# Kernel optimization log

Measured on AMD Instinct MI355X. Metric: run time of the kernel, lower is better.

The kernel has to match this reference:

```python
import jax, jax.numpy as jnp
import numpy as np

N = 50000          # nodes
E = 400000         # edges (before self-loops)
F_IN = 64          # node features
H = 256            # hidden_dim
HEADS = 8
HD = 32            # head dim (hidden_dim // 8)
L = 4              # num_layers
G = 64             # num graphs
NGF = 32           # graph features per graph
NC = 2             # classes
EPS = 1e-5


def _bn(x, g, b):
    # BatchNorm1d with batch statistics (training-mode math, no dropout)
    mu = jnp.mean(x, axis=0)
    var = jnp.var(x, axis=0)
    return (x - mu) * jax.lax.rsqrt(var + EPS) * g + b


def _gat(x, src, dst, W, a_src, a_dst, bias):
    # PyG GATConv math (self-loops already included in src/dst)
    h = (x @ W).reshape(N, HEADS, HD)                      # [N,8,32]
    as_n = jnp.sum(h * a_src, axis=-1)                     # [N,8]
    ad_n = jnp.sum(h * a_dst, axis=-1)                     # [N,8]
    e = jax.nn.leaky_relu(as_n[src] + ad_n[dst], 0.2)      # [E',8]
    m = jax.ops.segment_max(e, dst, num_segments=N)        # per-dest softmax
    ex = jnp.exp(e - m[dst])
    den = jax.ops.segment_sum(ex, dst, num_segments=N)
    alpha = ex / den[dst]                                  # [E',8]
    out = jax.ops.segment_sum(alpha[:, :, None] * h[src], dst, num_segments=N)
    return out.reshape(N, HEADS * HD) + bias


def setup_inputs() -> dict:
    key = jax.random.key(0)
    ks = jax.random.split(key, 20)
    s = 0.05
    inp = {
        "x": jax.random.normal(ks[0], (N, F_IN), jnp.float32),
        "edge_index": jax.random.randint(ks[1], (2, E), 0, N, jnp.int32),
        "batch": jnp.sort(jax.random.randint(ks[2], (N,), 0, G, jnp.int32)),
        "graph_features": jax.random.normal(ks[3], (G * NGF,), jnp.float32),
        # node encoder
        "W_enc": jax.random.normal(ks[4], (F_IN, H), jnp.float32) * s,
        "b_enc": jnp.zeros((H,), jnp.float32),
        "g_enc": jnp.ones((H,), jnp.float32),
        "be_enc": jnp.zeros((H,), jnp.float32),
        # GAT layers (stacked over L layers)
        "Wg": jax.random.normal(ks[5], (L, H, H), jnp.float32) * s,
        "att_src": jax.random.normal(ks[6], (L, HEADS, HD), jnp.float32) * s,
        "att_dst": jax.random.normal(ks[7], (L, HEADS, HD), jnp.float32) * s,
        "bg": jnp.zeros((L, H), jnp.float32),
        "bn_g": jnp.ones((L, H), jnp.float32),
        "bn_b": jnp.zeros((L, H), jnp.float32),
        # classifier: (3H + NGF) -> 2H -> H -> NC
        "W1": jax.random.normal(ks[8], (3 * H + NGF, 2 * H), jnp.float32) * s,
        "b1": jnp.zeros((2 * H,), jnp.float32),
        "g1": jnp.ones((2 * H,), jnp.float32),
        "be1": jnp.zeros((2 * H,), jnp.float32),
        "W2": jax.random.normal(ks[9], (2 * H, H), jnp.float32) * s,
        "b2": jnp.zeros((H,), jnp.float32),
        "g2": jnp.ones((H,), jnp.float32),
        "be2": jnp.zeros((H,), jnp.float32),
        "W3": jax.random.normal(ks[10], (H, NC), jnp.float32) * s,
        "b3": jnp.zeros((NC,), jnp.float32),
    }
    return inp


def reference(x, edge_index, batch, graph_features, W_enc, b_enc, g_enc, be_enc,
              Wg, att_src, att_dst, bg, bn_g, bn_b,
              W1, b1, g1, be1, W2, b2, g2, be2, W3, b3):
    gf = graph_features.reshape(G, NGF)
    # add self loops (PyG GATConv default)
    loop = jnp.arange(N, dtype=edge_index.dtype)
    src = jnp.concatenate([edge_index[0], loop])
    dst = jnp.concatenate([edge_index[1], loop])

    h = jax.nn.relu(_bn(x @ W_enc + b_enc, g_enc, be_enc))  # node encoder
    for i in range(L):
        h_in = h
        h = _gat(h, src, dst, Wg[i], att_src[i], att_dst[i], bg[i])
        h = jax.nn.relu(_bn(h, bn_g[i], bn_b[i]))
        if i > 0 and i % 2 == 0:
            h = h + h_in

    # concat pooling: mean / max / sum over graphs
    cnt = jax.ops.segment_sum(jnp.ones((N,), h.dtype), batch, num_segments=G)
    s = jax.ops.segment_sum(h, batch, num_segments=G)
    mean = s / cnt[:, None]
    mx = jax.ops.segment_max(h, batch, num_segments=G)
    pooled = jnp.concatenate([mean, mx, s], axis=1)         # [G, 3H]

    z = jnp.concatenate([pooled, gf], axis=1)               # [G, 3H+NGF]
    z = jax.nn.relu(_bn(z @ W1 + b1, g1, be1))
    z = jax.nn.relu(_bn(z @ W2 + b2, g2, be2))
    return z @ W3 + b3                                      # [G, NC]
```

## Files before the change

### kernel.cpp

```cpp
#include <hip/hip_runtime.h>

#define NN 50000
#define MPAD 50048
#define EE 400000
#define EP 450000
#define FIN 64
#define HH 256
#define GG 64
#define NGFD 32
#define SB 782
#define RB 64

typedef __attribute__((ext_vector_type(8))) _Float16 f16x8;
typedef __attribute__((ext_vector_type(8))) unsigned short u16x8;
typedef __attribute__((ext_vector_type(4))) float f32x4;

__device__ __forceinline__ unsigned short f2h(float f) {
  _Float16 h = (_Float16)f;
  return __builtin_bit_cast(unsigned short, h);
}
__device__ __forceinline__ float h2f(unsigned short s) {
  _Float16 h = __builtin_bit_cast(_Float16, s);
  return (float)h;
}

__global__ void k_init_deg(int* deg) {
  int i = blockIdx.x * 256 + threadIdx.x;
  if (i < NN) deg[i] = 1;
}
__global__ void k_hist(const int* __restrict__ dst, int* __restrict__ deg) {
  int e = blockIdx.x * 256 + threadIdx.x;
  if (e < EE) atomicAdd(&deg[dst[e]], 1);
}
__global__ void k_scan1(const int* __restrict__ deg, int* __restrict__ offs, int* __restrict__ aux) {
  __shared__ int sd[256];
  int b = blockIdx.x, t = threadIdx.x;
  int base = b * 1024 + t * 4;
  int v0 = 0, v1 = 0, v2 = 0, v3 = 0;
  if (base + 0 < NN) v0 = deg[base + 0];
  if (base + 1 < NN) v1 = deg[base + 1];
  if (base + 2 < NN) v2 = deg[base + 2];
  if (base + 3 < NN) v3 = deg[base + 3];
  sd[t] = v0 + v1 + v2 + v3;
  __syncthreads();
  for (int off = 1; off < 256; off <<= 1) {
    int x = (t >= off) ? sd[t - off] : 0;
    __syncthreads();
    sd[t] += x;
    __syncthreads();
  }
  if (t == 255) aux[b] = sd[255];
  int run = (t == 0) ? 0 : sd[t - 1];
  if (base + 0 < NN) offs[base + 0] = run; run += v0;
  if (base + 1 < NN) offs[base + 1] = run; run += v1;
  if (base + 2 < NN) offs[base + 2] = run; run += v2;
  if (base + 3 < NN) offs[base + 3] = run;
}
__global__ void k_scan2(int* aux, int nb) {
  if (threadIdx.x == 0 && blockIdx.x == 0) {
    int s = 0;
    for (int i = 0; i < nb; ++i) { int t = aux[i]; aux[i] = s; s += t; }
    aux[nb] = s;
  }
}
__global__ void k_scan3(int* __restrict__ offs, const int* __restrict__ aux) {
  int b = blockIdx.x, t = threadIdx.x;
  int base = b * 1024 + t * 4;
  int add = aux[b];
  #pragma unroll
  for (int i = 0; i < 4; ++i)
    if (base + i < NN) offs[base + i] += add;
  if (b == 0 && t == 0) offs[NN] = aux[gridDim.x];
}
__global__ void k_scatter(const int* __restrict__ srcA, const int* __restrict__ dstA,
                          int* __restrict__ cur, int* __restrict__ ssrc) {
  int e = blockIdx.x * 256 + threadIdx.x;
  if (e < EE) { int p = atomicAdd(&cur[dstA[e]], 1); ssrc[p] = srcA[e]; }
}
__global__ void k_scatter_self(int* __restrict__ cur, int* __restrict__ ssrc) {
  int i = blockIdx.x * 256 + threadIdx.x;
  if (i < NN) { int p = atomicAdd(&cur[i], 1); ssrc[p] = i; }
}

__global__ void k_bounds(const int* __restrict__ batch, int* __restrict__ start) {
  int g = threadIdx.x;
  if (g > GG) return;
  int lo = 0, hi = NN;
  while (lo < hi) { int mid = (lo + hi) >> 1; if (batch[mid] < g) lo = mid + 1; else hi = mid; }
  start[g] = lo;
}

__global__ void k_prepW(const float* __restrict__ W, unsigned short* __restrict__ WT, int K, int N) {
  __shared__ float tile[32][33];
  int l = blockIdx.z;
  const float* Wp = W + (size_t)l * K * N;
  unsigned short* Tp = WT + (size_t)l * K * N;
  int n0 = blockIdx.x * 32, k0 = blockIdx.y * 32;
  int tx = threadIdx.x & 31, ty = threadIdx.x >> 5;
  #pragma unroll
  for (int rr = 0; rr < 32; rr += 8) {
    int k = k0 + ty + rr, n = n0 + tx;
    if (k < K && n < N) tile[ty + rr][tx] = Wp[(size_t)k * N + n];
  }
  __syncthreads();
  #pragma unroll
  for (int rr = 0; rr < 32; rr += 8) {
    int n = n0 + ty + rr, k = k0 + tx;
    if (n < N && k < K) Tp[(size_t)n * K + k] = f2h(tile[tx][ty + rr]);
  }
}

__global__ void k_cvt_x(const float* __restrict__ x, unsigned short* __restrict__ xb) {
  size_t i = ((size_t)blockIdx.x * 256 + threadIdx.x) * 4;
  if (i >= (size_t)NN * FIN) return;
  float4 v = *reinterpret_cast<const float4*>(x + i);
  ushort4 o;
  o.x = f2h(v.x); o.y = f2h(v.y); o.z = f2h(v.z); o.w = f2h(v.w);
  *reinterpret_cast<ushort4*>(xb + i) = o;
}

__global__ __launch_bounds__(256) void k_mfma(const unsigned short* __restrict__ A,
                                              const unsigned short* __restrict__ BT,
                                              unsigned short* __restrict__ Cb, int K,
                                              const float* __restrict__ a_s,
                                              const float* __restrict__ a_d,
                                              float* __restrict__ asn,
                                              float* __restrict__ adn) {
  __shared__ unsigned short Tile[128 * 132];
  __shared__ float sas[128], sad[128];
  unsigned short* As = Tile;
  unsigned short* Bs = Tile + 8192;
  const int t = threadIdx.x;
  const int w = t >> 6, l = t & 63;
  const int row0 = blockIdx.x * 128;
  const int col0 = blockIdx.y * 128;
  const int wm = w & 1, wn = w >> 1;

  if (a_s && t < 128) {
    sas[t] = a_s[col0 + t];
    sad[t] = a_d[col0 + t];
  }

  f32x4 acc[4][4];
  #pragma unroll
  for (int i = 0; i < 4; ++i)
    #pragma unroll
    for (int j = 0; j < 4; ++j) acc[i][j] = (f32x4){0.f, 0.f, 0.f, 0.f};

  const int lrow = w * 8 + (l >> 3);
  const int ksrc_sh = ((l & 7) ^ (lrow & 7)) << 3;

  for (int k0 = 0; k0 < K; k0 += 64) {
    #pragma unroll
    for (int rd = 0; rd < 4; ++rd) {
      int r = rd * 32 + lrow;
      const unsigned short* ga = A + (size_t)(row0 + r) * K + k0 + ksrc_sh;
      __builtin_amdgcn_global_load_lds(
          (const __attribute__((address_space(1))) void*)ga,
          (__attribute__((address_space(3))) void*)(As + (size_t)(rd * 32 + w * 8) * 64),
          16, 0, 0);
    }
    #pragma unroll
    for (int rd = 0; rd < 4; ++rd) {
      int r = rd * 32 + lrow;
      const unsigned short* gb = BT + (size_t)(col0 + r) * K + k0 + ksrc_sh;
      __builtin_amdgcn_global_load_lds(
          (const __attribute__((address_space(1))) void*)gb,
          (__attribute__((address_space(3))) void*)(Bs + (size_t)(rd * 32 + w * 8) * 64),
          16, 0, 0);
    }
    __syncthreads();

    const char* AsB = (const char*)As;
    const char* BsB = (const char*)Bs;
    #pragma unroll
    for (int ks = 0; ks < 2; ++ks) {
      f16x8 af[4], bfr[4];
      #pragma unroll
      for (int i = 0; i < 4; ++i) {
        int ar = wm * 64 + i * 16 + (l & 15);
        int ab = ar * 128 + ((ks * 64 + (l >> 4) * 16) ^ ((ar & 7) << 4));
        af[i] = *(const f16x8*)(AsB + ab);
        int br = wn * 64 + i * 16 + (l & 15);
        int bb = br * 128 + ((ks * 64 + (l >> 4) * 16) ^ ((br & 7) << 4));
        bfr[i] = *(const f16x8*)(BsB + bb);
      }
      #pragma unroll
      for (int i = 0; i < 4; ++i)
        #pragma unroll
        for (int j = 0; j < 4; ++j)
          acc[i][j] = __builtin_amdgcn_mfma_f32_16x16x32_f16(af[i], bfr[j], acc[i][j], 0, 0, 0);
    }
    __syncthreads();
  }

  #pragma unroll
  for (int i = 0; i < 4; ++i) {
    int lrow2 = wm * 64 + i * 16 + ((l >> 4) * 4);
    #pragma unroll
    for (int j = 0; j < 4; ++j) {
      int lcol = wn * 64 + j * 16 + (l & 15);
      #pragma unroll
      for (int r = 0; r < 4; ++r)
        Tile[(lrow2 + r) * 132 + lcol] = f2h(acc[i][j][r]);
    }
  }
  __syncthreads();

  #pragma unroll
  for (int u = 0; u < 8; ++u) {
    int idx = u * 256 + t;
    int row = idx >> 4;
    int cc  = (idx & 15) * 8;
    int gr = row0 + row;
    if (gr < NN) {
      u16x8 v = *reinterpret_cast<const u16x8*>(&Tile[row * 132 + cc]);
      *reinterpret_cast<u16x8*>(Cb + (size_t)gr * HH + col0 + cc) = v;
    }
  }

  if (a_s) {
    int hbase = col0 >> 5;
    #pragma unroll
    for (int pp = 0; pp < 2; ++pp) {
      int p = pp * 256 + t;
      int row = p >> 2, hh = p & 3;
      int gr = row0 + row;
      if (gr < NN) {
        const unsigned short* rp = &Tile[row * 132 + hh * 32];
        const float* asp = &sas[hh * 32];
        const float* adp = &sad[hh * 32];
        float ps = 0.f, pd = 0.f;
        #pragma unroll
        for (int c = 0; c < 32; ++c) {
          float hv = h2f(rp[c]);
          ps += hv * asp[c];
          pd += hv * adp[c];
        }
        asn[gr * 8 + hbase + hh] = ps;
        adn[gr * 8 + hbase + hh] = pd;
      }
    }
  }
}

__global__ __launch_bounds__(256) void k_gat_agg(const int* __restrict__ offs, const int* __restrict__ ssrc,
                                                 const float* __restrict__ asn, const float* __restrict__ adn,
                                                 const unsigned short* __restrict__ hp,
                                                 unsigned short* __restrict__ outp) {
  int lane = threadIdx.x & 63;
  int n = blockIdx.x * 4 + (threadIdx.x >> 6);
  if (n >= NN) return;
  int hd = lane >> 3;
  float adh = adn[n * 8 + hd];
  int e0 = offs[n], e1 = offs[n + 1];
  float den = 0.f;
  float4 acc = make_float4(0.f, 0.f, 0.f, 0.f);

  auto step = [&](float av, ushort4 hv) {
    float e = fmaxf(av, 0.2f * av);
    float p = __expf(fminf(e, 40.f));
    den += p;
    acc.x += p * h2f(hv.x);
    acc.y += p * h2f(hv.y);
    acc.z += p * h2f(hv.z);
    acc.w += p * h2f(hv.w);
  };

  int k = e0;
  for (; k + 4 <= e1; k += 4) {
    int s0 = ssrc[k], s1 = ssrc[k + 1], s2 = ssrc[k + 2], s3 = ssrc[k + 3];
    ushort4 h0 = *reinterpret_cast<const ushort4*>(hp + (size_t)s0 * HH + lane * 4);
    ushort4 h1 = *reinterpret_cast<const ushort4*>(hp + (size_t)s1 * HH + lane * 4);
    ushort4 h2 = *reinterpret_cast<const ushort4*>(hp + (size_t)s2 * HH + lane * 4);
    ushort4 h3 = *reinterpret_cast<const ushort4*>(hp + (size_t)s3 * HH + lane * 4);
    float a0 = asn[s0 * 8 + hd] + adh;
    float a1 = asn[s1 * 8 + hd] + adh;
    float a2 = asn[s2 * 8 + hd] + adh;
    float a3 = asn[s3 * 8 + hd] + adh;
    step(a0, h0); step(a1, h1); step(a2, h2); step(a3, h3);
  }
  for (; k < e1; ++k) {
    int s = ssrc[k];
    ushort4 hv = *reinterpret_cast<const ushort4*>(hp + (size_t)s * HH + lane * 4);
    float av = asn[s * 8 + hd] + adh;
    step(av, hv);
  }
  float rden = 1.f / den;
  ushort4 o;
  o.x = f2h(acc.x * rden); o.y = f2h(acc.y * rden);
  o.z = f2h(acc.z * rden); o.w = f2h(acc.w * rden);
  *reinterpret_cast<ushort4*>(outp + (size_t)n * HH + lane * 4) = o;
}

__global__ void k_cstat_h(const unsigned short* __restrict__ x, float* __restrict__ pst) {
  int c = threadIdx.x, b = blockIdx.x;
  int r0 = b * 64, r1 = min(r0 + 64, NN);
  float s = 0.f, q = 0.f;
  for (int r = r0; r < r1; ++r) {
    float v = h2f(x[(size_t)r * HH + c]);
    s += v; q += v * v;
  }
  pst[b * 512 + c] = s;
  pst[b * 512 + 256 + c] = q;
}
__global__ void k_redstat1(const float* __restrict__ pst, float* __restrict__ pst2) {
  int t = threadIdx.x, p = blockIdx.x;
  int b0 = p * 13, b1 = min(b0 + 13, SB);
  float s0 = 0.f, s1 = 0.f;
  for (int b = b0; b < b1; ++b) {
    s0 += pst[b * 512 + t];
    s1 += pst[b * 512 + 256 + t];
  }
  pst2[p * 512 + t] = s0;
  pst2[p * 512 + 256 + t] = s1;
}
__global__ void k_redstat2(const float* __restrict__ pst2, float* __restrict__ stats) {
  int c = blockIdx.x * 256 + threadIdx.x;
  float s = 0.f;
  #pragma unroll
  for (int b = 0; b < RB; ++b) s += pst2[b * 512 + c];
  stats[c] = s;
}

__global__ void k_bnap_h(const unsigned short* __restrict__ x, const float* __restrict__ stats,
                         const float* __restrict__ g, const float* __restrict__ b,
                         const unsigned short* res, unsigned short* __restrict__ ybf) {
  size_t i = ((size_t)blockIdx.x * 256 + threadIdx.x) * 4;
  if (i >= (size_t)NN * HH) return;
  ushort4 v = *reinterpret_cast<const ushort4*>(x + i);
  int c = (int)(i & 255);
  const float invN = 1.f / (float)NN;
  float vv[4] = {h2f(v.x), h2f(v.y), h2f(v.z), h2f(v.w)};
  float rv[4] = {0.f, 0.f, 0.f, 0.f};
  if (res) {
    ushort4 r4 = *reinterpret_cast<const ushort4*>(res + i);
    rv[0] = h2f(r4.x); rv[1] = h2f(r4.y); rv[2] = h2f(r4.z); rv[3] = h2f(r4.w);
  }
  float o[4];
  #pragma unroll
  for (int j = 0; j < 4; ++j) {
    int cc = c + j;
    float mean = stats[cc] * invN;
    float var = stats[HH + cc] * invN - mean * mean;
    float rs = rsqrtf(var + 1e-5f);
    float val = (vv[j] - mean) * rs * g[cc] + b[cc];
    val = fmaxf(val, 0.f) + rv[j];
    o[j] = val;
  }
  ushort4 bo;
  bo.x = f2h(o[0]); bo.y = f2h(o[1]); bo.z = f2h(o[2]); bo.w = f2h(o[3]);
  *reinterpret_cast<ushort4*>(ybf + i) = bo;
}

__global__ void k_pool(const unsigned short* __restrict__ h, const int* __restrict__ batch,
                       float* __restrict__ gsum, float* __restrict__ gmax) {
  int c = threadIdx.x;
  int r0 = blockIdx.x * 64, r1 = min(r0 + 64, NN);
  if (r0 >= r1) return;
  int curg = batch[r0];
  float s = 0.f, mx = 0.f;
  for (int r = r0; r < r1; ++r) {
    int g = batch[r];
    if (g != curg) {
      atomicAdd(&gsum[curg * HH + c], s);
      atomicMax((int*)&gmax[curg * HH + c], __float_as_int(mx));
      s = 0.f; mx = 0.f; curg = g;
    }
    float v = h2f(h[(size_t)r * HH + c]);
    s += v; mx = fmaxf(mx, v);
  }
  atomicAdd(&gsum[curg * HH + c], s);
  atomicMax((int*)&gmax[curg * HH + c], __float_as_int(mx));
}
__global__ void k_buildz(const float* __restrict__ gsum, const float* __restrict__ gmax,
                         const int* __restrict__ start, const float* __restrict__ gf,
                         float* __restrict__ z) {
  int g = blockIdx.x;
  float invc = 1.f / (float)(start[g + 1] - start[g]);
  for (int c = threadIdx.x; c < 800; c += 256) {
    float v;
    if (c < 256)      v = gsum[g * HH + c] * invc;
    else if (c < 512) v = gmax[g * HH + (c - 256)];
    else if (c < 768) v = gsum[g * HH + (c - 512)];
    else              v = gf[g * NGFD + (c - 768)];
    z[g * 800 + c] = v;
  }
}

__global__ __launch_bounds__(256) void k_linsplit(const float* __restrict__ zin,
                                                  const float* __restrict__ W,
                                                  float* __restrict__ pacc, int K, int OC) {
  __shared__ float zs[64][65];
  int t = threadIdx.x;
  int kc = blockIdx.y, k0 = kc * 64;
  int kmax = min(64, K - k0);
  for (int idx = t; idx < 64 * 64; idx += 256) {
    int r = idx >> 6, k = idx & 63;
    zs[r][k] = (k < kmax) ? zin[(size_t)r * K + k0 + k] : 0.f;
  }
  __syncthreads();
  int jl = t & 15, rq = t >> 4;
  int j = blockIdx.x * 16 + jl;
  float acc[4] = {0.f, 0.f, 0.f, 0.f};
  int k = 0;
  for (; k + 8 <= kmax; k += 8) {
    float wv[8];
    #pragma unroll
    for (int u = 0; u < 8; ++u) wv[u] = W[(size_t)(k0 + k + u) * OC + j];
    #pragma unroll
    for (int u = 0; u < 8; ++u)
      #pragma unroll
      for (int rr = 0; rr < 4; ++rr) acc[rr] += zs[rq * 4 + rr][k + u] * wv[u];
  }
  for (; k < kmax; ++k) {
    float wv = W[(size_t)(k0 + k) * OC + j];
    #pragma unroll
    for (int rr = 0; rr < 4; ++rr) acc[rr] += zs[rq * 4 + rr][k] * wv;
  }
  float* pp = pacc + ((size_t)kc * OC + j) * 64 + rq * 4;
  #pragma unroll
  for (int rr = 0; rr < 4; ++rr) pp[rr] = acc[rr];
}

__global__ __launch_bounds__(64) void k_linred(const float* __restrict__ pacc,
                                               const float* __restrict__ g,
                                               const float* __restrict__ be,
                                               float* __restrict__ zout, int OC, int KC) {
  int j = blockIdx.x, r = threadIdx.x;
  float s = 0.f;
  for (int kc = 0; kc < KC; ++kc) s += pacc[((size_t)kc * OC + j) * 64 + r];
  float S = s, Q = s * s;
  #pragma unroll
  for (int off = 32; off >= 1; off >>= 1) {
    S += __shfl_xor(S, off);
    Q += __shfl_xor(Q, off);
  }
  float mu = S * (1.f / 64.f);
  float var = Q * (1.f / 64.f) - mu * mu;
  float scv = rsqrtf(var + 1e-5f) * g[j];
  float sh = be[j] - mu * scv;
  zout[(size_t)r * OC + j] = fmaxf(s * scv + sh, 0.f);
}

__global__ void k_final(const float* __restrict__ z2, const float* __restrict__ W3,
                        const float* __restrict__ b3, float* __restrict__ out) {
  int t = threadIdx.x;
  if (t >= 128) return;
  int i = t >> 1, j = t & 1;
  float acc = b3[j];
  for (int k = 0; k < 256; ++k) acc += z2[i * 256 + k] * W3[k * 2 + j];
  out[i * 2 + j] = acc;
}

extern "C" void kernel_launch(void* const* d_in, const int* in_sizes, int n_in,
                              void* d_out, int out_size, void* d_ws, size_t ws_size,
                              hipStream_t stream) {
  const float* x      = (const float*)d_in[0];
  const int*   ei     = (const int*)d_in[1];
  const int*   batch  = (const int*)d_in[2];
  const float* gf     = (const float*)d_in[3];
  const float* W_enc  = (const float*)d_in[4];
  const float* g_enc  = (const float*)d_in[6];
  const float* be_enc = (const float*)d_in[7];
  const float* Wg     = (const float*)d_in[8];
  const float* att_s  = (const float*)d_in[9];
  const float* att_d  = (const float*)d_in[10];
  const float* bn_g   = (const float*)d_in[12];
  const float* bn_b   = (const float*)d_in[13];
  const float* W1     = (const float*)d_in[14];
  const float* g1     = (const float*)d_in[16];
  const float* be1    = (const float*)d_in[17];
  const float* W2     = (const float*)d_in[18];
  const float* g2     = (const float*)d_in[20];
  const float* be2    = (const float*)d_in[21];
  const float* W3     = (const float*)d_in[22];
  const float* b3     = (const float*)d_in[23];
  float* out = (float*)d_out;

  char* w = (char*)d_ws;
  auto alloc = [&](size_t bytes) { char* p = w; w += (bytes + 255) & ~(size_t)255; return p; };
  unsigned short* Cc_h = (unsigned short*)alloc((size_t)MPAD * HH * 2);
  unsigned short* A_bf = (unsigned short*)alloc((size_t)MPAD * HH * 2);
  unsigned short* hp   = (unsigned short*)alloc((size_t)MPAD * HH * 2);
  unsigned short* x_bf = (unsigned short*)alloc((size_t)MPAD * FIN * 2);
  float* asn  = (float*)alloc((size_t)NN * 8 * 4);
  float* adn  = (float*)alloc((size_t)NN * 8 * 4);
  int*   deg  = (int*)alloc((size_t)NN * 4);
  int*   offs = (int*)alloc((size_t)(NN + 1) * 4);
  int*   cur  = (int*)alloc((size_t)NN * 4);
  int*   ssrc = (int*)alloc((size_t)EP * 4);
  float* pst  = (float*)alloc((size_t)SB * 512 * 4);
  float* pst2 = (float*)alloc((size_t)RB * 512 * 4);
  float* stats= (float*)alloc(512 * 4);
  int*   aux  = (int*)alloc(64 * 4);
  int*   start= (int*)alloc(65 * 4);
  unsigned short* WencT = (unsigned short*)alloc((size_t)HH * FIN * 2);
  unsigned short* WgT   = (unsigned short*)alloc((size_t)4 * HH * HH * 2);
  float* gsum = (float*)alloc((size_t)GG * HH * 4);
  float* gmax = (float*)alloc((size_t)GG * HH * 4);
  float* zb   = (float*)alloc((size_t)GG * 800 * 4);
  float* z1   = (float*)alloc((size_t)GG * 512 * 4);
  float* z2   = (float*)alloc((size_t)GG * 256 * 4);
  float* pacc = (float*)alloc((size_t)13 * 512 * 64 * 4);

  const int* e_src = ei;
  const int* e_dst = ei + EE;

  k_init_deg<<<196, 256, 0, stream>>>(deg);
  k_hist<<<1563, 256, 0, stream>>>(e_dst, deg);
  k_scan1<<<49, 256, 0, stream>>>(deg, offs, aux);
  k_scan2<<<1, 64, 0, stream>>>(aux, 49);
  k_scan3<<<49, 256, 0, stream>>>(offs, aux);
  hipMemcpyAsync(cur, offs, (size_t)NN * 4, hipMemcpyDeviceToDevice, stream);
  k_scatter<<<1563, 256, 0, stream>>>(e_src, e_dst, cur, ssrc);
  k_scatter_self<<<196, 256, 0, stream>>>(cur, ssrc);
  k_bounds<<<1, 128, 0, stream>>>(batch, start);

  k_prepW<<<dim3(8, 2, 1), 256, 0, stream>>>(W_enc, WencT, FIN, HH);
  k_prepW<<<dim3(8, 8, 4), 256, 0, stream>>>(Wg, WgT, HH, HH);
  k_cvt_x<<<3125, 256, 0, stream>>>(x, x_bf);

  dim3 mg(MPAD / 128, 2);

  k_mfma<<<mg, 256, 0, stream>>>(x_bf, WencT, hp, FIN, nullptr, nullptr, nullptr, nullptr);
  k_cstat_h<<<SB, 256, 0, stream>>>(hp, pst);
  k_redstat1<<<RB, 256, 0, stream>>>(pst, pst2);
  k_redstat2<<<2, 256, 0, stream>>>(pst2, stats);
  k_bnap_h<<<12500, 256, 0, stream>>>(hp, stats, g_enc, be_enc, nullptr, A_bf);

  for (int l = 0; l < 4; ++l) {
    k_mfma<<<mg, 256, 0, stream>>>(A_bf, WgT + (size_t)l * HH * HH, hp, HH,
                                   att_s + l * HH, att_d + l * HH, asn, adn);
    k_gat_agg<<<12500, 256, 0, stream>>>(offs, ssrc, asn, adn, hp, Cc_h);
    k_cstat_h<<<SB, 256, 0, stream>>>(Cc_h, pst);
    k_redstat1<<<RB, 256, 0, stream>>>(pst, pst2);
    k_redstat2<<<2, 256, 0, stream>>>(pst2, stats);
    k_bnap_h<<<12500, 256, 0, stream>>>(Cc_h, stats, bn_g + l * HH, bn_b + l * HH,
                                        (l == 2) ? A_bf : nullptr, A_bf);
  }

  hipMemsetAsync(gsum, 0, (size_t)GG * HH * 4, stream);
  hipMemsetAsync(gmax, 0, (size_t)GG * HH * 4, stream);
  k_pool<<<SB, 256, 0, stream>>>(A_bf, batch, gsum, gmax);
  k_buildz<<<GG, 256, 0, stream>>>(gsum, gmax, start, gf, zb);
  k_linsplit<<<dim3(32, 13), 256, 0, stream>>>(zb, W1, pacc, 800, 512);
  k_linred<<<512, 64, 0, stream>>>(pacc, g1, be1, z1, 512, 13);
  k_linsplit<<<dim3(16, 8), 256, 0, stream>>>(z1, W2, pacc, 512, 256);
  k_linred<<<256, 64, 0, stream>>>(pacc, g2, be2, z2, 256, 8);
  k_final<<<1, 128, 0, stream>>>(z2, W3, b3, out);
}
```

Measured before the change: 585.6 us.

## Split each node's GAT edge aggregation across two wavefronts with LDS reduction

The GAT aggregation kernel now assigns two wavefronts per destination node, each handling half of the incoming edge list, and combines partial numerators and denominators through shared memory before normalizing and writing fp16 output. The goal is more memory-level parallelism and shorter per-wave dependency chains for the gather-bound aggregation. The cost is a block-wide barrier, extra LDS traffic and doubled block size. With an average degree near 9, each half has few edges, so the unrolled-by-4 loop runs less often.

```diff
diff --git a/kernel.cpp b/kernel.cpp
--- a/kernel.cpp
+++ b/kernel.cpp
@@ -244,53 +244,80 @@
   }
 }
 
-__global__ __launch_bounds__(256) void k_gat_agg(const int* __restrict__ offs, const int* __restrict__ ssrc,
+__global__ __launch_bounds__(512) void k_gat_agg(const int* __restrict__ offs, const int* __restrict__ ssrc,
                                                  const float* __restrict__ asn, const float* __restrict__ adn,
                                                  const unsigned short* __restrict__ hp,
                                                  unsigned short* __restrict__ outp) {
-  int lane = threadIdx.x & 63;
-  int n = blockIdx.x * 4 + (threadIdx.x >> 6);
-  if (n >= NN) return;
-  int hd = lane >> 3;
-  float adh = adn[n * 8 + hd];
-  int e0 = offs[n], e1 = offs[n + 1];
+  __shared__ float part[8][256];
+  __shared__ float sden[8];
+  int t = threadIdx.x;
+  int wv = t >> 6, lane = t & 63;
+  int nd = wv >> 1, sub = wv & 1;
+  int n = blockIdx.x * 4 + nd;
   float den = 0.f;
   float4 acc = make_float4(0.f, 0.f, 0.f, 0.f);
 
-  auto step = [&](float av, ushort4 hv) {
-    float e = fmaxf(av, 0.2f * av);
-    float p = __expf(fminf(e, 40.f));
-    den += p;
-    acc.x += p * h2f(hv.x);
-    acc.y += p * h2f(hv.y);
-    acc.z += p * h2f(hv.z);
-    acc.w += p * h2f(hv.w);
-  };
-
-  int k = e0;
-  for (; k + 4 <= e1; k += 4) {
-    int s0 = ssrc[k], s1 = ssrc[k + 1], s2 = ssrc[k + 2], s3 = ssrc[k + 3];
-    ushort4 h0 = *reinterpret_cast<const ushort4*>(hp + (size_t)s0 * HH + lane * 4);
-    ushort4 h1 = *reinterpret_cast<const ushort4*>(hp + (size_t)s1 * HH + lane * 4);
-    ushort4 h2 = *reinterpret_cast<const ushort4*>(hp + (size_t)s2 * HH + lane * 4);
-    ushort4 h3 = *reinterpret_cast<const ushort4*>(hp + (size_t)s3 * HH + lane * 4);
-    float a0 = asn[s0 * 8 + hd] + adh;
-    float a1 = asn[s1 * 8 + hd] + adh;
-    float a2 = asn[s2 * 8 + hd] + adh;
-    float a3 = asn[s3 * 8 + hd] + adh;
-    step(a0, h0); step(a1, h1); step(a2, h2); step(a3, h3);
-  }
-  for (; k < e1; ++k) {
-    int s = ssrc[k];
-    ushort4 hv = *reinterpret_cast<const ushort4*>(hp + (size_t)s * HH + lane * 4);
-    float av = asn[s * 8 + hd] + adh;
-    step(av, hv);
-  }
-  float rden = 1.f / den;
-  ushort4 o;
-  o.x = f2h(acc.x * rden); o.y = f2h(acc.y * rden);
-  o.z = f2h(acc.z * rden); o.w = f2h(acc.w * rden);
-  *reinterpret_cast<ushort4*>(outp + (size_t)n * HH + lane * 4) = o;
+  if (n < NN) {
+    int hd = lane >> 3;
+    float adh = adn[n * 8 + hd];
+    int e0 = offs[n], e1 = offs[n + 1];
+    int cnt = e1 - e0;
+    int mid = e0 + ((cnt + 1) >> 1);
+    int ka = sub ? mid : e0;
+    int kb = sub ? e1 : mid;
+
+    auto step = [&](float av, ushort4 hv) {
+      float e = fmaxf(av, 0.2f * av);
+      float p = __expf(fminf(e, 40.f));
+      den += p;
+      acc.x += p * h2f(hv.x);
+      acc.y += p * h2f(hv.y);
+      acc.z += p * h2f(hv.z);
+      acc.w += p * h2f(hv.w);
+    };
+
+    int k = ka;
+    for (; k + 4 <= kb; k += 4) {
+      int s0 = ssrc[k], s1 = ssrc[k + 1], s2 = ssrc[k + 2], s3 = ssrc[k + 3];
+      ushort4 h0 = *reinterpret_cast<const ushort4*>(hp + (size_t)s0 * HH + lane * 4);
+      ushort4 h1 = *reinterpret_cast<const ushort4*>(hp + (size_t)s1 * HH + lane * 4);
+      ushort4 h2 = *reinterpret_cast<const ushort4*>(hp + (size_t)s2 * HH + lane * 4);
+      ushort4 h3 = *reinterpret_cast<const ushort4*>(hp + (size_t)s3 * HH + lane * 4);
+      float a0 = asn[s0 * 8 + hd] + adh;
+      float a1 = asn[s1 * 8 + hd] + adh;
+      float a2 = asn[s2 * 8 + hd] + adh;
+      float a3 = asn[s3 * 8 + hd] + adh;
+      step(a0, h0); step(a1, h1); step(a2, h2); step(a3, h3);
+    }
+    for (; k < kb; ++k) {
+      int s = ssrc[k];
+      ushort4 hv = *reinterpret_cast<const ushort4*>(hp + (size_t)s * HH + lane * 4);
+      float av = asn[s * 8 + hd] + adh;
+      step(av, hv);
+    }
+  }
+
+  part[wv][lane * 4 + 0] = acc.x;
+  part[wv][lane * 4 + 1] = acc.y;
+  part[wv][lane * 4 + 2] = acc.z;
+  part[wv][lane * 4 + 3] = acc.w;
+  __shared__ float dpart[8][8];
+  if ((lane & 7) == 0) dpart[wv][lane >> 3] = den;
+  __syncthreads();
+
+  int nd2 = t >> 7;
+  int cl = (t & 127) * 2;
+  int n2 = blockIdx.x * 4 + nd2;
+  if (n2 < NN) {
+    int hd2 = cl >> 5;
+    float dtot = dpart[nd2 * 2][hd2] + dpart[nd2 * 2 + 1][hd2];
+    float r = 1.f / dtot;
+    float c0 = (part[nd2 * 2][cl] + part[nd2 * 2 + 1][cl]) * r;
+    float c1 = (part[nd2 * 2][cl + 1] + part[nd2 * 2 + 1][cl + 1]) * r;
+    ushort2 o;
+    o.x = f2h(c0); o.y = f2h(c1);
+    *reinterpret_cast<ushort2*>(outp + (size_t)n2 * HH + cl) = o;
+  }
 }
 
 __global__ void k_cstat_h(const unsigned short* __restrict__ x, float* __restrict__ pst) {
@@ -532,7 +559,7 @@
   for (int l = 0; l < 4; ++l) {
     k_mfma<<<mg, 256, 0, stream>>>(A_bf, WgT + (size_t)l * HH * HH, hp, HH,
                                    att_s + l * HH, att_d + l * HH, asn, adn);
-    k_gat_agg<<<12500, 256, 0, stream>>>(offs, ssrc, asn, adn, hp, Cc_h);
+    k_gat_agg<<<12500, 512, 0, stream>>>(offs, ssrc, asn, adn, hp, Cc_h);
     k_cstat_h<<<SB, 256, 0, stream>>>(Cc_h, pst);
     k_redstat1<<<RB, 256, 0, stream>>>(pst, pst2);
     k_redstat2<<<2, 256, 0, stream>>>(pst2, stats);
```

Result: slower. 633.1 us (+8.1%).
